# Kernel tuning notes

Hardware: AMD Instinct MI355X
Metric: run time of the kernel (lower is better)

Reference implementation:

```python
import jax, jax.numpy as jnp
import numpy as np

N_NODES = 30000
N_EDGES = 480000
NEG_SLOPE = 0.2  # PyG GATConv default negative_slope


def setup_inputs() -> dict:
    key = jax.random.key(0)
    ks = jax.random.split(key, 10)

    def glorot(k, shape, fan):
        return jax.random.normal(k, shape, jnp.float32) * (1.0 / np.sqrt(fan))

    x = jax.random.normal(ks[0], (N_NODES, 1024), jnp.float32)
    edge_index = jax.random.randint(ks[1], (2, N_EDGES), 0, N_NODES)
    # layer 1: in=1024 -> heads=8, C=64, concat -> 512
    W1 = glorot(ks[2], (1024, 512), 1024)
    a1_src = glorot(ks[3], (8, 64), 64)
    a1_dst = glorot(ks[4], (8, 64), 64)
    b1 = jnp.zeros((512,), jnp.float32)
    # layer 2: in=512 -> heads=1, C=256, no concat
    W2 = glorot(ks[5], (512, 256), 512)
    a2_src = glorot(ks[6], (1, 256), 256)
    a2_dst = glorot(ks[7], (1, 256), 256)
    b2 = jnp.zeros((256,), jnp.float32)
    return {"x": x, "edge_index": edge_index, "W1": W1, "a1_src": a1_src,
            "a1_dst": a1_dst, "b1": b1, "W2": W2, "a2_src": a2_src,
            "a2_dst": a2_dst, "b2": b2}


def gat_conv(x, src, dst, W, a_src, a_dst, bias, heads, channels, concat):
    """PyG-style GATConv (self-loops already included in src/dst)."""
    n = x.shape[0]
    h = (x @ W).reshape(n, heads, channels)          # [N, H, C]
    al_s = jnp.einsum('nhc,hc->nh', h, a_src)        # per-node src logits
    al_d = jnp.einsum('nhc,hc->nh', h, a_dst)        # per-node dst logits
    e = jax.nn.leaky_relu(al_s[src] + al_d[dst], NEG_SLOPE)   # [E, H]
    # segment softmax over edges grouped by destination node
    m = jax.ops.segment_max(e, dst, num_segments=n)
    p = jnp.exp(e - m[dst])
    s = jax.ops.segment_sum(p, dst, num_segments=n)
    alpha = p / s[dst]                               # [E, H]
    out = jax.ops.segment_sum(alpha[:, :, None] * h[src], dst, num_segments=n)
    out = out.reshape(n, heads * channels) if concat else out.mean(axis=1)
    return out + bias


def reference(x, edge_index, W1, a1_src, a1_dst, b1, W2, a2_src, a2_dst, b2):
    n = x.shape[0]
    loops = jnp.arange(n, dtype=edge_index.dtype)
    src = jnp.concatenate([edge_index[0], loops])    # add self-loops (PyG default)
    dst = jnp.concatenate([edge_index[1], loops])
    # eval mode: dropout is identity
    h = jax.nn.elu(gat_conv(x, src, dst, W1, a1_src, a1_dst, b1, 8, 64, True))
    out = gat_conv(h, src, dst, W2, a2_src, a2_dst, b2, 1, 256, False)
    return out
```

## Files before the change

### kernel.cpp

```cpp
#include <hip/hip_runtime.h>
#include <hip/hip_bf16.h>

typedef unsigned int uint;
typedef unsigned short ushort;
typedef __attribute__((ext_vector_type(8))) short short8;
typedef __attribute__((ext_vector_type(4))) short short4v;
typedef __attribute__((ext_vector_type(4))) float f32x4;

#define LEAKY 0.2f

__device__ __forceinline__ ushort f2bf(float f) {
  __hip_bfloat16 h = __float2bfloat16(f);
  return __builtin_bit_cast(ushort, h);
}
__device__ __forceinline__ float bf2f(ushort u) {
  uint v = ((uint)u) << 16;
  return __builtin_bit_cast(float, v);
}
__device__ __forceinline__ void gload_lds16(const void* g, void* l) {
  __builtin_amdgcn_global_load_lds(
      (const __attribute__((address_space(1))) void*)g,
      (__attribute__((address_space(3))) void*)l, 16, 0, 0);
}

__global__ void convw(const float* __restrict__ W, ushort* __restrict__ Wt,
                      int K, int N) {
  int idx = blockIdx.x * 256 + threadIdx.x;
  if (idx >= K * N) return;
  int nrow = idx / K;
  int k = idx - nrow * K;
  Wt[idx] = f2bf(W[(size_t)k * N + nrow]);
}

__global__ void zero2(int* a, int* b, int n) {
  int i = blockIdx.x * 256 + threadIdx.x;
  if (i < n) { a[i] = 0; b[i] = 0; }
}

__global__ void hist(const int* __restrict__ dst, int E, int n, int* cnt) {
  int e = blockIdx.x * 256 + threadIdx.x;
  if (e >= E + n) return;
  int d = (e < E) ? dst[e] : (e - E);
  atomicAdd(&cnt[d], 1);
}

__global__ __launch_bounds__(1024) void scan_fast(const int* __restrict__ cnt,
                                                  int* __restrict__ rp, int n) {
  __shared__ int wsum[16];
  __shared__ int woff[16];
  const int t = threadIdx.x;
  const int per = (n + 1023) / 1024;
  const int base = t * per;
  int local[32];
  int s = 0;
#pragma unroll
  for (int i = 0; i < 32; i++) {
    if (i >= per) break;
    int idx = base + i;
    int v = (idx < n) ? cnt[idx] : 0;
    local[i] = s;
    s += v;
  }
  const int lane = t & 63, wave = t >> 6;
  int incl = s;
#pragma unroll
  for (int off = 1; off < 64; off <<= 1) {
    int v = __shfl_up(incl, off);
    if (lane >= off) incl += v;
  }
  if (lane == 63) wsum[wave] = incl;
  __syncthreads();
  if (wave == 0 && lane < 16) {
    int v = wsum[lane];
    int wi = v;
#pragma unroll
    for (int off = 1; off < 16; off <<= 1) {
      int u = __shfl_up(wi, off);
      if (lane >= off) wi += u;
    }
    woff[lane] = wi - v;
  }
  __syncthreads();
  const int gexcl = woff[wave] + (incl - s);
#pragma unroll
  for (int i = 0; i < 32; i++) {
    if (i >= per) break;
    int idx = base + i;
    if (idx < n) rp[idx] = gexcl + local[i];
  }
  if (t == 1023) rp[n] = woff[15] + incl;
}

__global__ void scatter(const int* __restrict__ src, const int* __restrict__ dst,
                        int E, int n, const int* __restrict__ rp,
                        int* fill, int* __restrict__ csr) {
  int e = blockIdx.x * 256 + threadIdx.x;
  if (e >= E + n) return;
  int s, d;
  if (e < E) { s = src[e]; d = dst[e]; } else { s = d = e - E; }
  int pos = rp[d] + atomicAdd(&fill[d], 1);
  csr[pos] = s;
}

template <int ABYTES>
__global__ __launch_bounds__(512) void gemm_bd(
    const void* __restrict__ Av, const ushort* __restrict__ Bt,
    ushort* __restrict__ C, int M, int K, int N) {
  constexpr int BM = 128, BN = 256, BK = 32;
  constexpr int SPRA = (BK * ABYTES) / 16;
  constexpr int A_ITER = (BM * SPRA) / 512;
  __shared__ __align__(16) char As[BM * BK * ABYTES];
  const int tid = threadIdx.x;
  const int wave = tid >> 6, lane = tid & 63;
  const int g = lane >> 4, r16 = lane & 15;
  const int nby = N / BN;
  const int bx = (int)blockIdx.x / nby;
  const int by = (int)blockIdx.x - bx * nby;
  const int bm = bx * BM, bn = by * BN;
  const int wm = (wave >> 2) * 64, wn = (wave & 3) * 64;

  f32x4 acc[4][4] = {};
  const char* A = (const char*)Av;

  for (int k0 = 0; k0 < K; k0 += BK) {
#pragma unroll
    for (int i = 0; i < A_ITER; i++) {
      int slot = i * 512 + tid;
      int row = slot / SPRA;
      int cp = slot - row * SPRA;
      int key = (ABYTES == 4) ? (row & 7) : ((row >> 1) & 3);
      int cl = cp ^ key;
      int arow = bm + row;
      arow = arow < M ? arow : M - 1;
      const char* gp = A + ((size_t)arow * K + k0) * ABYTES + cl * 16;
      char* lp = As + (i * 512 + wave * 64) * 16;
      gload_lds16(gp, lp);
    }
    asm volatile("s_waitcnt vmcnt(0)" ::: "memory");
    __syncthreads();

    short8 bfr[4];
#pragma unroll
    for (int ni = 0; ni < 4; ni++) {
      int row = bn + wn + ni * 16 + r16;
      bfr[ni] = *(const short8*)(Bt + (size_t)row * K + k0 + g * 8);
    }

    short8 af[4];
#pragma unroll
    for (int mi = 0; mi < 4; mi++) {
      int row = wm + mi * 16 + r16;
      if constexpr (ABYTES == 4) {
        int key = row & 7;
        f32x4 lo = *(const f32x4*)(As + (row * 8 + ((2 * g) ^ key)) * 16);
        f32x4 hi = *(const f32x4*)(As + (row * 8 + ((2 * g + 1) ^ key)) * 16);
        short8 s;
#pragma unroll
        for (int qq = 0; qq < 4; qq++) {
          s[qq] = (short)f2bf(lo[qq]);
          s[qq + 4] = (short)f2bf(hi[qq]);
        }
        af[mi] = s;
      } else {
        int key = (row >> 1) & 3;
        af[mi] = *(const short8*)(As + (row * 4 + (g ^ key)) * 16);
      }
    }
#pragma unroll
    for (int mi = 0; mi < 4; mi++)
#pragma unroll
      for (int ni = 0; ni < 4; ni++)
        acc[mi][ni] = __builtin_amdgcn_mfma_f32_16x16x32_bf16(
            af[mi], bfr[ni], acc[mi][ni], 0, 0, 0);
    __syncthreads();
  }

#pragma unroll
  for (int mi = 0; mi < 4; mi++) {
#pragma unroll
    for (int j = 0; j < 4; j++) {
      int row = bm + wm + mi * 16 + g * 4 + j;
      if (row < M) {
#pragma unroll
        for (int ni = 0; ni < 4; ni++) {
          int col = bn + wn + ni * 16 + r16;
          C[(size_t)row * N + col] = f2bf(acc[mi][ni][j]);
        }
      }
    }
  }
}

__global__ void logits1(const ushort* __restrict__ h1, const float* __restrict__ a_s,
                        const float* __restrict__ a_d, float* __restrict__ al_s,
                        float* __restrict__ al_d, int n) {
  int node = blockIdx.x * 4 + (threadIdx.x >> 6);
  if (node >= n) return;
  int lane = threadIdx.x & 63;
  int c0 = lane * 8;
  short8 hv = *(const short8*)&h1[(size_t)node * 512 + c0];
  float ps = 0.f, pd = 0.f;
#pragma unroll
  for (int j = 0; j < 8; j++) {
    float f = bf2f((ushort)hv[j]);
    ps += f * a_s[c0 + j];
    pd += f * a_d[c0 + j];
  }
#pragma unroll
  for (int m = 1; m < 8; m <<= 1) {
    ps += __shfl_xor(ps, m);
    pd += __shfl_xor(pd, m);
  }
  if ((lane & 7) == 0) {
    al_s[node * 8 + (lane >> 3)] = ps;
    al_d[node * 8 + (lane >> 3)] = pd;
  }
}

__global__ void logits2(const ushort* __restrict__ h2, const float* __restrict__ a_s,
                        const float* __restrict__ a_d, float* __restrict__ al_s,
                        float* __restrict__ al_d, int n) {
  int node = blockIdx.x * 4 + (threadIdx.x >> 6);
  if (node >= n) return;
  int lane = threadIdx.x & 63;
  int c0 = lane * 4;
  short4v hv = *(const short4v*)&h2[(size_t)node * 256 + c0];
  float ps = 0.f, pd = 0.f;
#pragma unroll
  for (int j = 0; j < 4; j++) {
    float f = bf2f((ushort)hv[j]);
    ps += f * a_s[c0 + j];
    pd += f * a_d[c0 + j];
  }
#pragma unroll
  for (int m = 1; m < 64; m <<= 1) {
    ps += __shfl_xor(ps, m);
    pd += __shfl_xor(pd, m);
  }
  if (lane == 0) {
    al_s[node] = ps;
    al_d[node] = pd;
  }
}

__global__ void agg1(const int* __restrict__ rp, const int* __restrict__ csr,
                     const ushort* __restrict__ h1, const float* __restrict__ al_s,
                     const float* __restrict__ al_d, const float* __restrict__ b1,
                     ushort* __restrict__ h2in, int n) {
  int node = blockIdx.x * 4 + (threadIdx.x >> 6);
  if (node >= n) return;
  int lane = threadIdx.x & 63;
  int head = lane >> 3, c0 = lane * 8;
  float ad = al_d[node * 8 + head];
  int beg = rp[node], end = rp[node + 1];
  float sum = 0.f;
  float acc[8] = {};
  int j = beg;
  for (; j + 4 <= end; j += 4) {
    int s0 = csr[j], s1 = csr[j + 1], s2 = csr[j + 2], s3 = csr[j + 3];
    float e0 = al_s[s0 * 8 + head] + ad;
    float e1 = al_s[s1 * 8 + head] + ad;
    float e2 = al_s[s2 * 8 + head] + ad;
    float e3 = al_s[s3 * 8 + head] + ad;
    short8 v0 = *(const short8*)&h1[(size_t)s0 * 512 + c0];
    short8 v1 = *(const short8*)&h1[(size_t)s1 * 512 + c0];
    short8 v2 = *(const short8*)&h1[(size_t)s2 * 512 + c0];
    short8 v3 = *(const short8*)&h1[(size_t)s3 * 512 + c0];
    e0 = e0 > 0.f ? e0 : LEAKY * e0;
    e1 = e1 > 0.f ? e1 : LEAKY * e1;
    e2 = e2 > 0.f ? e2 : LEAKY * e2;
    e3 = e3 > 0.f ? e3 : LEAKY * e3;
    float p0 = __expf(e0), p1 = __expf(e1), p2 = __expf(e2), p3 = __expf(e3);
    sum += (p0 + p1) + (p2 + p3);
#pragma unroll
    for (int qq = 0; qq < 8; qq++)
      acc[qq] += p0 * bf2f((ushort)v0[qq]) + p1 * bf2f((ushort)v1[qq]) +
                 p2 * bf2f((ushort)v2[qq]) + p3 * bf2f((ushort)v3[qq]);
  }
  for (; j < end; j++) {
    int s = csr[j];
    float e = al_s[s * 8 + head] + ad;
    e = e > 0.f ? e : LEAKY * e;
    float p = __expf(e);
    sum += p;
    short8 hv = *(const short8*)&h1[(size_t)s * 512 + c0];
#pragma unroll
    for (int qq = 0; qq < 8; qq++) acc[qq] += p * bf2f((ushort)hv[qq]);
  }
  float inv = 1.0f / sum;
  short8 o;
#pragma unroll
  for (int qq = 0; qq < 8; qq++) {
    float rr = acc[qq] * inv + b1[c0 + qq];
    rr = rr > 0.f ? rr : (__expf(rr) - 1.0f);
    o[qq] = (short)f2bf(rr);
  }
  *(short8*)&h2in[(size_t)node * 512 + c0] = o;
}

__global__ void agg2(const int* __restrict__ rp, const int* __restrict__ csr,
                     const ushort* __restrict__ h2, const float* __restrict__ al_s,
                     const float* __restrict__ al_d, const float* __restrict__ b2,
                     float* __restrict__ out, int n) {
  int node = blockIdx.x * 4 + (threadIdx.x >> 6);
  if (node >= n) return;
  int lane = threadIdx.x & 63;
  int c0 = lane * 4;
  float ad = al_d[node];
  int beg = rp[node], end = rp[node + 1];
  float sum = 0.f;
  float a0 = 0.f, a1 = 0.f, a2 = 0.f, a3 = 0.f;
  int j = beg;
  for (; j + 4 <= end; j += 4) {
    int s0 = csr[j], s1 = csr[j + 1], s2 = csr[j + 2], s3 = csr[j + 3];
    float e0 = al_s[s0] + ad;
    float e1 = al_s[s1] + ad;
    float e2 = al_s[s2] + ad;
    float e3 = al_s[s3] + ad;
    short4v v0 = *(const short4v*)&h2[(size_t)s0 * 256 + c0];
    short4v v1 = *(const short4v*)&h2[(size_t)s1 * 256 + c0];
    short4v v2 = *(const short4v*)&h2[(size_t)s2 * 256 + c0];
    short4v v3 = *(const short4v*)&h2[(size_t)s3 * 256 + c0];
    e0 = e0 > 0.f ? e0 : LEAKY * e0;
    e1 = e1 > 0.f ? e1 : LEAKY * e1;
    e2 = e2 > 0.f ? e2 : LEAKY * e2;
    e3 = e3 > 0.f ? e3 : LEAKY * e3;
    float p0 = __expf(e0), p1 = __expf(e1), p2 = __expf(e2), p3 = __expf(e3);
    sum += (p0 + p1) + (p2 + p3);
    a0 += p0 * bf2f((ushort)v0[0]) + p1 * bf2f((ushort)v1[0]) +
          p2 * bf2f((ushort)v2[0]) + p3 * bf2f((ushort)v3[0]);
    a1 += p0 * bf2f((ushort)v0[1]) + p1 * bf2f((ushort)v1[1]) +
          p2 * bf2f((ushort)v2[1]) + p3 * bf2f((ushort)v3[1]);
    a2 += p0 * bf2f((ushort)v0[2]) + p1 * bf2f((ushort)v1[2]) +
          p2 * bf2f((ushort)v2[2]) + p3 * bf2f((ushort)v3[2]);
    a3 += p0 * bf2f((ushort)v0[3]) + p1 * bf2f((ushort)v1[3]) +
          p2 * bf2f((ushort)v2[3]) + p3 * bf2f((ushort)v3[3]);
  }
  for (; j < end; j++) {
    int s = csr[j];
    float e = al_s[s] + ad;
    e = e > 0.f ? e : LEAKY * e;
    float p = __expf(e);
    sum += p;
    short4v hv = *(const short4v*)&h2[(size_t)s * 256 + c0];
    a0 += p * bf2f((ushort)hv[0]);
    a1 += p * bf2f((ushort)hv[1]);
    a2 += p * bf2f((ushort)hv[2]);
    a3 += p * bf2f((ushort)hv[3]);
  }
  float inv = 1.0f / sum;
  f32x4 o;
  o[0] = a0 * inv + b2[c0 + 0];
  o[1] = a1 * inv + b2[c0 + 1];
  o[2] = a2 * inv + b2[c0 + 2];
  o[3] = a3 * inv + b2[c0 + 3];
  *(f32x4*)&out[(size_t)node * 256 + c0] = o;
}

extern "C" void kernel_launch(void* const* d_in, const int* in_sizes, int n_in,
                              void* d_out, int out_size, void* d_ws, size_t ws_size,
                              hipStream_t stream) {
  const float* x = (const float*)d_in[0];
  const int* ei = (const int*)d_in[1];
  const float* W1 = (const float*)d_in[2];
  const float* a1s = (const float*)d_in[3];
  const float* a1d = (const float*)d_in[4];
  const float* b1 = (const float*)d_in[5];
  const float* W2 = (const float*)d_in[6];
  const float* a2s = (const float*)d_in[7];
  const float* a2d = (const float*)d_in[8];
  const float* b2 = (const float*)d_in[9];
  float* out = (float*)d_out;

  const int n = in_sizes[0] / 1024;
  const int E = in_sizes[1] / 2;
  const int K1 = 1024, C1 = 512, C2 = 256;

  char* ws = (char*)d_ws;
  ushort* h1 = (ushort*)(ws + 0);
  ushort* h2in = (ushort*)(ws + 31000000);
  ushort* h2 = (ushort*)(ws + 62000000);
  float* al_s = (float*)(ws + 78000000);
  float* al_d = (float*)(ws + 79000000);
  float* al2s = (float*)(ws + 80000000);
  float* al2d = (float*)(ws + 80200000);
  ushort* W1t = (ushort*)(ws + 80400000);
  ushort* W2t = (ushort*)(ws + 81600000);
  int* cnt = (int*)(ws + 82000000);
  int* rp = (int*)(ws + 82200000);
  int* fill = (int*)(ws + 82400000);
  int* csr = (int*)(ws + 82600000);

  const int* esrc = ei;
  const int* edst = ei + E;
  const int ET = E + n;

  convw<<<(C1 * K1 + 255) / 256, 256, 0, stream>>>(W1, W1t, K1, C1);
  convw<<<(C2 * C1 + 255) / 256, 256, 0, stream>>>(W2, W2t, C1, C2);
  zero2<<<(n + 255) / 256, 256, 0, stream>>>(cnt, fill, n);
  hist<<<(ET + 255) / 256, 256, 0, stream>>>(edst, E, n, cnt);
  scan_fast<<<1, 1024, 0, stream>>>(cnt, rp, n);
  scatter<<<(ET + 255) / 256, 256, 0, stream>>>(esrc, edst, E, n, rp, fill, csr);

  const int gx1 = ((n + 127) / 128) * (C1 / 256);
  gemm_bd<4><<<gx1, 512, 0, stream>>>(x, W1t, h1, n, K1, C1);
  logits1<<<(n + 3) / 4, 256, 0, stream>>>(h1, a1s, a1d, al_s, al_d, n);
  agg1<<<(n + 3) / 4, 256, 0, stream>>>(rp, csr, h1, al_s, al_d, b1, h2in, n);

  const int gx2 = ((n + 127) / 128) * (C2 / 256);
  gemm_bd<2><<<gx2, 512, 0, stream>>>(h2in, W2t, h2, n, C1, C2);
  logits2<<<(n + 3) / 4, 256, 0, stream>>>(h2, a2s, a2d, al2s, al2d, n);
  agg2<<<(n + 3) / 4, 256, 0, stream>>>(rp, csr, h2, al2s, al2d, b2, out, n);
}
```

Baseline: 320.5 us.

## Fuse attention logit computation into GEMM epilogue and stage B tiles in LDS

Attention logits (al_s, al_d) are now computed in the epilogue of both projection GEMMs from the fp32 accumulators, which removes the separate logits1/logits2 kernels and their re-read of h. The GEMM also stages the B (weight) tile into swizzled LDS with global_load_lds instead of loading it directly from global memory into registers, and the two weight-conversion launches are merged into one. In exchange the GEMM uses more LDS and does a cross-lane and cross-wave reduction in its epilogue. The logits are also now taken from unrounded fp32 accumulators rather than bf16 h, which changes the numerics slightly.

```diff
diff --git a/kernel.cpp b/kernel.cpp
--- a/kernel.cpp
+++ b/kernel.cpp
@@ -23,13 +23,20 @@
       (__attribute__((address_space(3))) void*)l, 16, 0, 0);
 }
 
-__global__ void convw(const float* __restrict__ W, ushort* __restrict__ Wt,
-                      int K, int N) {
+__global__ void convw_all(const float* __restrict__ W1, ushort* __restrict__ W1t,
+                          const float* __restrict__ W2, ushort* __restrict__ W2t) {
   int idx = blockIdx.x * 256 + threadIdx.x;
-  if (idx >= K * N) return;
-  int nrow = idx / K;
-  int k = idx - nrow * K;
-  Wt[idx] = f2bf(W[(size_t)k * N + nrow]);
+  const int n1 = 512 * 1024;
+  if (idx < n1) {
+    int nrow = idx >> 10, k = idx & 1023;
+    W1t[idx] = f2bf(W1[(size_t)k * 512 + nrow]);
+  } else {
+    idx -= n1;
+    if (idx < 256 * 512) {
+      int nrow = idx >> 9, k = idx & 511;
+      W2t[idx] = f2bf(W2[(size_t)k * 256 + nrow]);
+    }
+  }
 }
 
 __global__ void zero2(int* a, int* b, int n) {
@@ -102,14 +109,17 @@
   csr[pos] = s;
 }
 
-template <int ABYTES>
-__global__ __launch_bounds__(512) void gemm_bd(
+template <int ABYTES, int HEADS>
+__global__ __launch_bounds__(512) void gemm_fl(
     const void* __restrict__ Av, const ushort* __restrict__ Bt,
-    ushort* __restrict__ C, int M, int K, int N) {
+    ushort* __restrict__ C, float* __restrict__ al_s, float* __restrict__ al_d,
+    const float* __restrict__ as_vec, const float* __restrict__ ad_vec,
+    int M, int K, int N) {
   constexpr int BM = 128, BN = 256, BK = 32;
   constexpr int SPRA = (BK * ABYTES) / 16;
   constexpr int A_ITER = (BM * SPRA) / 512;
   __shared__ __align__(16) char As[BM * BK * ABYTES];
+  __shared__ __align__(16) char Bs[BN * BK * 2];
   const int tid = threadIdx.x;
   const int wave = tid >> 6, lane = tid & 63;
   const int g = lane >> 4, r16 = lane & 15;
@@ -136,17 +146,20 @@
       char* lp = As + (i * 512 + wave * 64) * 16;
       gload_lds16(gp, lp);
     }
+#pragma unroll
+    for (int i = 0; i < 2; i++) {
+      int slot = i * 512 + tid;
+      int row = slot >> 2;
+      int cp = slot & 3;
+      int cl = cp ^ ((row >> 1) & 3);
+      const char* gp = (const char*)(Bt + (size_t)(bn + row) * K + k0 + cl * 8);
+      char* lp = Bs + (i * 512 + wave * 64) * 16;
+      gload_lds16(gp, lp);
+    }
     asm volatile("s_waitcnt vmcnt(0)" ::: "memory");
     __syncthreads();
 
-    short8 bfr[4];
-#pragma unroll
-    for (int ni = 0; ni < 4; ni++) {
-      int row = bn + wn + ni * 16 + r16;
-      bfr[ni] = *(const short8*)(Bt + (size_t)row * K + k0 + g * 8);
-    }
-
-    short8 af[4];
+    short8 af[4], bfr[4];
 #pragma unroll
     for (int mi = 0; mi < 4; mi++) {
       int row = wm + mi * 16 + r16;
@@ -167,6 +180,12 @@
       }
     }
 #pragma unroll
+    for (int ni = 0; ni < 4; ni++) {
+      int row = wn + ni * 16 + r16;
+      int key = (row >> 1) & 3;
+      bfr[ni] = *(const short8*)(Bs + (row * 4 + (g ^ key)) * 16);
+    }
+#pragma unroll
     for (int mi = 0; mi < 4; mi++)
 #pragma unroll
       for (int ni = 0; ni < 4; ni++)
@@ -189,57 +208,85 @@
       }
     }
   }
-}
-
-__global__ void logits1(const ushort* __restrict__ h1, const float* __restrict__ a_s,
-                        const float* __restrict__ a_d, float* __restrict__ al_s,
-                        float* __restrict__ al_d, int n) {
-  int node = blockIdx.x * 4 + (threadIdx.x >> 6);
-  if (node >= n) return;
-  int lane = threadIdx.x & 63;
-  int c0 = lane * 8;
-  short8 hv = *(const short8*)&h1[(size_t)node * 512 + c0];
-  float ps = 0.f, pd = 0.f;
-#pragma unroll
-  for (int j = 0; j < 8; j++) {
-    float f = bf2f((ushort)hv[j]);
-    ps += f * a_s[c0 + j];
-    pd += f * a_d[c0 + j];
-  }
-#pragma unroll
-  for (int m = 1; m < 8; m <<= 1) {
-    ps += __shfl_xor(ps, m);
-    pd += __shfl_xor(pd, m);
-  }
-  if ((lane & 7) == 0) {
-    al_s[node * 8 + (lane >> 3)] = ps;
-    al_d[node * 8 + (lane >> 3)] = pd;
-  }
-}
-
-__global__ void logits2(const ushort* __restrict__ h2, const float* __restrict__ a_s,
-                        const float* __restrict__ a_d, float* __restrict__ al_s,
-                        float* __restrict__ al_d, int n) {
-  int node = blockIdx.x * 4 + (threadIdx.x >> 6);
-  if (node >= n) return;
-  int lane = threadIdx.x & 63;
-  int c0 = lane * 4;
-  short4v hv = *(const short4v*)&h2[(size_t)node * 256 + c0];
-  float ps = 0.f, pd = 0.f;
-#pragma unroll
-  for (int j = 0; j < 4; j++) {
-    float f = bf2f((ushort)hv[j]);
-    ps += f * a_s[c0 + j];
-    pd += f * a_d[c0 + j];
-  }
-#pragma unroll
-  for (int m = 1; m < 64; m <<= 1) {
-    ps += __shfl_xor(ps, m);
-    pd += __shfl_xor(pd, m);
-  }
-  if (lane == 0) {
-    al_s[node] = ps;
-    al_d[node] = pd;
+
+  if constexpr (HEADS == 8) {
+    const int head = (bn + wn) >> 6;
+    float asr[4], adr[4];
+#pragma unroll
+    for (int ni = 0; ni < 4; ni++) {
+      asr[ni] = as_vec[head * 64 + ni * 16 + r16];
+      adr[ni] = ad_vec[head * 64 + ni * 16 + r16];
+    }
+#pragma unroll
+    for (int mi = 0; mi < 4; mi++) {
+#pragma unroll
+      for (int j = 0; j < 4; j++) {
+        float ps = 0.f, pd = 0.f;
+#pragma unroll
+        for (int ni = 0; ni < 4; ni++) {
+          ps += acc[mi][ni][j] * asr[ni];
+          pd += acc[mi][ni][j] * adr[ni];
+        }
+#pragma unroll
+        for (int off = 1; off < 16; off <<= 1) {
+          ps += __shfl_xor(ps, off);
+          pd += __shfl_xor(pd, off);
+        }
+        if (r16 == 0) {
+          int row = bm + wm + mi * 16 + g * 4 + j;
+          if (row < M) {
+            al_s[row * 8 + head] = ps;
+            al_d[row * 8 + head] = pd;
+          }
+        }
+      }
+    }
+  } else {
+    float* sred = (float*)As;
+    float* dred = sred + 512;
+    float asr[4], adr[4];
+#pragma unroll
+    for (int ni = 0; ni < 4; ni++) {
+      asr[ni] = as_vec[wn + ni * 16 + r16];
+      adr[ni] = ad_vec[wn + ni * 16 + r16];
+    }
+    __syncthreads();
+#pragma unroll
+    for (int mi = 0; mi < 4; mi++) {
+#pragma unroll
+      for (int j = 0; j < 4; j++) {
+        float ps = 0.f, pd = 0.f;
+#pragma unroll
+        for (int ni = 0; ni < 4; ni++) {
+          ps += acc[mi][ni][j] * asr[ni];
+          pd += acc[mi][ni][j] * adr[ni];
+        }
+#pragma unroll
+        for (int off = 1; off < 16; off <<= 1) {
+          ps += __shfl_xor(ps, off);
+          pd += __shfl_xor(pd, off);
+        }
+        if (r16 == 0) {
+          int rloc = mi * 16 + g * 4 + j;
+          sred[wave * 64 + rloc] = ps;
+          dred[wave * 64 + rloc] = pd;
+        }
+      }
+    }
+    __syncthreads();
+    if (tid < 128) {
+      int base = (tid >= 64) ? 4 : 0;
+      int rl = tid & 63;
+      float s = sred[(base + 0) * 64 + rl] + sred[(base + 1) * 64 + rl] +
+                sred[(base + 2) * 64 + rl] + sred[(base + 3) * 64 + rl];
+      float d = dred[(base + 0) * 64 + rl] + dred[(base + 1) * 64 + rl] +
+                dred[(base + 2) * 64 + rl] + dred[(base + 3) * 64 + rl];
+      int row = bm + tid;
+      if (row < M) {
+        al_s[row] = s;
+        al_d[row] = d;
+      }
+    }
   }
 }
 
@@ -395,20 +442,17 @@
   const int* edst = ei + E;
   const int ET = E + n;
 
-  convw<<<(C1 * K1 + 255) / 256, 256, 0, stream>>>(W1, W1t, K1, C1);
-  convw<<<(C2 * C1 + 255) / 256, 256, 0, stream>>>(W2, W2t, C1, C2);
+  convw_all<<<(C1 * K1 + C2 * C1 + 255) / 256, 256, 0, stream>>>(W1, W1t, W2, W2t);
   zero2<<<(n + 255) / 256, 256, 0, stream>>>(cnt, fill, n);
   hist<<<(ET + 255) / 256, 256, 0, stream>>>(edst, E, n, cnt);
   scan_fast<<<1, 1024, 0, stream>>>(cnt, rp, n);
   scatter<<<(ET + 255) / 256, 256, 0, stream>>>(esrc, edst, E, n, rp, fill, csr);
 
   const int gx1 = ((n + 127) / 128) * (C1 / 256);
-  gemm_bd<4><<<gx1, 512, 0, stream>>>(x, W1t, h1, n, K1, C1);
-  logits1<<<(n + 3) / 4, 256, 0, stream>>>(h1, a1s, a1d, al_s, al_d, n);
+  gemm_fl<4, 8><<<gx1, 512, 0, stream>>>(x, W1t, h1, al_s, al_d, a1s, a1d, n, K1, C1);
   agg1<<<(n + 3) / 4, 256, 0, stream>>>(rp, csr, h1, al_s, al_d, b1, h2in, n);
 
   const int gx2 = ((n + 127) / 128) * (C2 / 256);
-  gemm_bd<2><<<gx2, 512, 0, stream>>>(h2in, W2t, h2, n, C1, C2);
-  logits2<<<(n + 3) / 4, 256, 0, stream>>>(h2, a2s, a2d, al2s, al2d, n);
+  gemm_fl<2, 1><<<gx2, 512, 0, stream>>>(h2in, W2t, h2, al2s, al2d, a2s, a2d, n, C1, C2);
   agg2<<<(n + 3) / 4, 256, 0, stream>>>(rp, csr, h2, al2s, al2d, b2, out, n);
 }
```

New measurement: 272.7 us. 1.18x faster.
